# Optimization experiments

Hardware: AMD Instinct MI355X
Metric: run time of the kernel (lower is better)

Reference implementation:

```python
import jax, jax.numpy as jnp
import numpy as np

N, F, D = 32, 1024, 512
H = 2 * D  # dim * ratio
EPS = 1e-5


def batchnorm1d(x, gamma, beta):
    # x: (N, F, L); BatchNorm1d over channel dim F, stats over (N, L) (training mode, biased var)
    mean = jnp.mean(x, axis=(0, 2), keepdims=True)
    var = jnp.var(x, axis=(0, 2), keepdims=True)
    xn = (x - mean) * jax.lax.rsqrt(var + EPS)
    return xn * gamma[None, :, None] + beta[None, :, None]


def setup_inputs() -> dict:
    key = jax.random.key(0)
    ks = jax.random.split(key, 5)
    x = jax.random.normal(ks[0], (N, F, D), dtype=jnp.float32)
    W0 = jax.random.normal(ks[1], (H, D), dtype=jnp.float32) * 0.02  # Linear(D->H) weight (out,in)
    b0 = jnp.zeros((H,), jnp.float32)
    W1 = jax.random.normal(ks[2], (D, H), dtype=jnp.float32) * 0.02  # Linear(H->D)
    b1 = jnp.zeros((D,), jnp.float32)
    Wc = jax.random.normal(ks[3], (F, F), dtype=jnp.float32) * 0.02  # Conv1d k=1 weight (out_ch,in_ch)
    bc = jnp.zeros((F,), jnp.float32)
    ones = jnp.ones((F,), jnp.float32)
    zeros = jnp.zeros((F,), jnp.float32)
    return {
        "x": x,
        "W0": W0, "b0": b0, "g0": ones, "be0": zeros,
        "W1": W1, "b1": b1, "g1": ones, "be1": zeros,
        "gf": ones, "bf": zeros,
        "Wc": Wc, "bc": bc,
        "go": ones, "bo": zeros,
    }


def reference(x, W0, b0, g0, be0, W1, b1, g1, be1, gf, bf, Wc, bc, go, bo):
    # proj_mlp0: Linear(D->H) + BN1d(F)
    v = jnp.einsum('nfd,hd->nfh', x, W0) + b0  # (N, F, H)
    v = batchnorm1d(v, g0, be0)
    # correlation: bmm(v, v^T) -> softsign -> bmm(w, v)
    w = jnp.einsum('nfh,ngh->nfg', v, v)  # (N, F, F)
    w = w / (1.0 + jnp.abs(w))  # softsign
    v = jnp.einsum('nfg,ngh->nfh', w, v)  # (N, F, H)
    # proj_mlp1: Linear(H->D) + BN1d(F)
    v = jnp.einsum('nfh,dh->nfd', v, W1) + b1  # (N, F, D)
    v = batchnorm1d(v, g1, be1)
    # feed_norm(v + x)
    xr = batchnorm1d(v + x, gf, bf)
    # proj_conv: Conv1d(F->F, kernel=1) over channel dim
    v = jnp.einsum('oi,nid->nod', Wc, xr) + bc[None, :, None]
    return batchnorm1d(v + xr, go, bo)
```

## Files before the change

### kernel.cpp

```cpp
#include <hip/hip_runtime.h>
#include <stdint.h>

#define NB 32
#define FC 1024
#define DD 512
#define HH 1024
#define BN_EPS 1e-5f

typedef unsigned short u16;
typedef unsigned int u32;
typedef __attribute__((ext_vector_type(8))) short bf16x8;
typedef __attribute__((ext_vector_type(4))) float f32x4;
typedef __attribute__((ext_vector_type(8))) unsigned short ushort8v;

#define AS1 __attribute__((address_space(1)))
#define AS3 __attribute__((address_space(3)))

__device__ __forceinline__ float b2f(u16 u) {
    union { u32 i; float f; } v;
    v.i = ((u32)u) << 16;
    return v.f;
}
__device__ __forceinline__ u16 f2b(float f) {
    union { float f; u32 i; } v;
    v.f = f;
    const u32 b = v.i;
    return (u16)((b + 0x7FFFu + ((b >> 16) & 1u)) >> 16);
}

__device__ __forceinline__ void gld16(const u16* g, u16* l) {
    __builtin_amdgcn_global_load_lds((const AS1 u32*)g, (AS3 u32*)l, 16, 0, 0);
}

__device__ __forceinline__ void swizzle_tiles(int& mt, int& nt, int& zt) {
    const int gx = gridDim.x, gy = gridDim.y, gz = gridDim.z;
    const int mzTot = gy * gz;
    if ((mzTot & 7) != 0) { nt = blockIdx.x; mt = blockIdx.y; zt = blockIdx.z; return; }
    long lin = ((long)blockIdx.z * gy + blockIdx.y) * gx + blockIdx.x;
    const int slab = mzTot >> 3;
    const int xcd = (int)(lin & 7);
    const long idx = lin >> 3;
    nt = (int)(idx % gx);
    const int mz = (int)(idx / gx) + xcd * slab;
    mt = mz % gy;
    zt = mz / gy;
}

__global__ __launch_bounds__(256) void init_detect(
    float* __restrict__ sp, const u32* __restrict__ x, int* __restrict__ flag)
{
    sp[blockIdx.x * 256 + threadIdx.x] = 0.0f;
    if (blockIdx.x != 0) return;
    __shared__ int cnt[256];
    int c = 0;
    for (int i = threadIdx.x; i < 4096; i += 256) {
        const u32 lo = x[i] & 0xFFFFu;
        const u32 e = (lo >> 7) & 0xFFu;
        if (e >= 0x68u && e <= 0x85u) c++;
    }
    cnt[threadIdx.x] = c;
    __syncthreads();
    for (int s = 128; s > 0; s >>= 1) {
        if (threadIdx.x < (unsigned)s) cnt[threadIdx.x] += cnt[threadIdx.x + s];
        __syncthreads();
    }
    if (threadIdx.x == 0) flag[0] = (cnt[0] > 2048) ? 1 : 0;
}

__global__ __launch_bounds__(256) void fold_bn(
    const float* __restrict__ sp, const u16* __restrict__ gamma,
    const u16* __restrict__ beta, float* __restrict__ ssf, float invCnt)
{
    const int f = blockIdx.x * 256 + threadIdx.x;
    if (f < FC) {
        const float mean = sp[f] * invCnt;
        const float var  = sp[FC + f] * invCnt - mean * mean;
        const float rstd = rsqrtf(var + BN_EPS);
        const float sc   = b2f(gamma[f]) * rstd;
        ssf[f]      = sc;
        ssf[FC + f] = b2f(beta[f]) - mean * sc;
    }
}

__global__ __launch_bounds__(256) void convert_to_bf16(
    const void* __restrict__ src, u16* __restrict__ dst, long n4,
    const int* __restrict__ flag)
{
    const bool isbf = (*flag != 0);
    long i4 = (long)blockIdx.x * blockDim.x + threadIdx.x;
    const long stride = (long)gridDim.x * blockDim.x;
    for (; i4 < n4; i4 += stride) {
        const long i = i4 << 2;
        if (isbf) {
            *(ushort4*)(dst + i) = *(const ushort4*)((const u16*)src + i);
        } else {
            const float4 v = *(const float4*)((const float*)src + i);
            ushort4 o;
            o.x = f2b(v.x); o.y = f2b(v.y); o.z = f2b(v.z); o.w = f2b(v.w);
            *(ushort4*)(dst + i) = o;
        }
    }
}

struct ConvArgs { const void* src[14]; long off[14]; long n4[14]; };
__global__ __launch_bounds__(256) void convert_params(
    ConvArgs a, u16* __restrict__ dst, const int* __restrict__ flag)
{
    const bool isbf = (*flag != 0);
    const long stride = (long)gridDim.x * blockDim.x;
    for (int s = 0; s < 14; ++s) {
        const long n4 = a.n4[s];
        u16* d = dst + a.off[s];
        const void* sp = a.src[s];
        for (long i4 = (long)blockIdx.x * blockDim.x + threadIdx.x; i4 < n4;
             i4 += stride) {
            const long i = i4 << 2;
            if (isbf) {
                *(ushort4*)(d + i) = *(const ushort4*)((const u16*)sp + i);
            } else {
                const float4 v = *(const float4*)((const float*)sp + i);
                ushort4 o;
                o.x = f2b(v.x); o.y = f2b(v.y); o.z = f2b(v.z); o.w = f2b(v.w);
                *(ushort4*)(d + i) = o;
            }
        }
    }
}

template<bool BIAS, bool SOFTSIGN, bool STATS, bool RESID>
__global__ __launch_bounds__(512, 4) void gemm128x256_nt(
    const u16* __restrict__ A, const u16* __restrict__ B,
    const u16* __restrict__ bias, const u16* __restrict__ resid,
    u16* __restrict__ C, float* __restrict__ sp,
    int M, int N, int K, int lda, int ldb, int ldc,
    long sA, long sB, long sC)
{
    extern __shared__ char smem[];

    int mt, nt, zt;
    swizzle_tiles(mt, nt, zt);
    const u16* Ab = A + (long)zt * sA + (long)(mt * 128) * lda;
    const u16* Bb = B + (long)zt * sB + (long)(nt * 256) * ldb;
    C += (long)zt * sC;
    const u16* RP = RESID ? (resid + (long)zt * sC) : nullptr;

    const int tid  = threadIdx.x;
    const int lane = tid & 63;
    const int wv   = tid >> 6;
    const int wrr  = (wv >> 2) * 64;
    const int wc   = (wv & 3) * 64;
    const int lm   = lane & 15;
    const int q    = lane >> 4;

    int aOff[4], bOff[4];
    #pragma unroll
    for (int i = 0; i < 4; ++i) {
        const int r = wrr + i * 16 + lm;
        aOff[i] = r * 64 + ((q ^ ((r >> 1) & 3)) << 4);
    }
    #pragma unroll
    for (int j = 0; j < 4; ++j) {
        const int r = wc + j * 16 + lm;
        bOff[j] = r * 64 + ((q ^ ((r >> 1) & 3)) << 4);
    }

    const int rw = lane >> 2, qs = lane & 3;
    const int rA  = wv * 16 + rw;
    const int rB0 = wv * 32 + rw;
    const int rB1 = wv * 32 + 16 + rw;
    const u16* pA  = Ab + (long)rA  * lda + ((qs ^ ((rA  >> 1) & 3)) << 3);
    const u16* pB0 = Bb + (long)rB0 * ldb + ((qs ^ ((rB0 >> 1) & 3)) << 3);
    const u16* pB1 = Bb + (long)rB1 * ldb + ((qs ^ ((rB1 >> 1) & 3)) << 3);
    const int ldsA  = wv * 1024;
    const int ldsB0 = wv * 2048;
    const int ldsB1 = wv * 2048 + 1024;

#define STAGE(bufOff, kofs) { \
    gld16(pA  + (kofs), (u16*)(smem + (bufOff) + ldsA)); \
    gld16(pB0 + (kofs), (u16*)(smem + (bufOff) + 8192 + ldsB0)); \
    gld16(pB1 + (kofs), (u16*)(smem + (bufOff) + 8192 + ldsB1)); }

    f32x4 acc[4][4] = {};

    const int NT = K >> 5;

    STAGE(0, 0);
    __syncthreads();

    for (int t = 0; t < NT; ++t) {
        const int bo = (t & 1) * 24576;
        const int bn = ((t + 1) & 1) * 24576;
        if (t + 1 < NT) STAGE(bn, (t + 1) * 32);

        bf16x8 a[4], b[4];
        const char* baseA = smem + bo;
        const char* baseB = smem + bo + 8192;
        #pragma unroll
        for (int i = 0; i < 4; ++i) a[i] = *(const bf16x8*)(baseA + aOff[i]);
        #pragma unroll
        for (int j = 0; j < 4; ++j) b[j] = *(const bf16x8*)(baseB + bOff[j]);

        #pragma unroll
        for (int i = 0; i < 4; ++i)
            #pragma unroll
            for (int j = 0; j < 4; ++j)
                acc[i][j] = __builtin_amdgcn_mfma_f32_16x16x32_bf16(
                    a[i], b[j], acc[i][j], 0, 0, 0);

        __syncthreads();
    }

#undef STAGE

    float* rep = (float*)smem + wv * (16 * 65);
    const int rr = lane >> 2;
    const int cg = lane & 3;
    const int m0 = mt * 128;
    const int n0 = nt * 256;
    #pragma unroll
    for (int i = 0; i < 4; ++i) {
        #pragma unroll
        for (int j = 0; j < 4; ++j) {
            const int col = 16 * j + lm;
            const float bj = BIAS ? b2f(bias[n0 + wc + col]) : 0.0f;
            #pragma unroll
            for (int r = 0; r < 4; ++r) {
                float v = acc[i][j][r] + bj;
                if (SOFTSIGN) v = v / (1.0f + fabsf(v));
                rep[(q * 4 + r) * 65 + col] = v;
            }
        }
        const int row = m0 + wrr + 16 * i + rr;
        const float* lr = rep + rr * 65 + cg * 16;
        float4 f0 = *(const float4*)(lr + 0);
        float4 f1 = *(const float4*)(lr + 4);
        float4 f2 = *(const float4*)(lr + 8);
        float4 f3 = *(const float4*)(lr + 12);
        if (RESID) {
            const u16* rp = RP + (long)row * ldc + n0 + wc + cg * 16;
            const ushort8v ra = *(const ushort8v*)rp;
            const ushort8v rb = *(const ushort8v*)(rp + 8);
            f0.x += b2f(ra[0]); f0.y += b2f(ra[1]); f0.z += b2f(ra[2]); f0.w += b2f(ra[3]);
            f1.x += b2f(ra[4]); f1.y += b2f(ra[5]); f1.z += b2f(ra[6]); f1.w += b2f(ra[7]);
            f2.x += b2f(rb[0]); f2.y += b2f(rb[1]); f2.z += b2f(rb[2]); f2.w += b2f(rb[3]);
            f3.x += b2f(rb[4]); f3.y += b2f(rb[5]); f3.z += b2f(rb[6]); f3.w += b2f(rb[7]);
        }
        if (STATS) {
            float s1 = (f0.x + f0.y + f0.z + f0.w) + (f1.x + f1.y + f1.z + f1.w)
                     + (f2.x + f2.y + f2.z + f2.w) + (f3.x + f3.y + f3.z + f3.w);
            float s2 = f0.x*f0.x + f0.y*f0.y + f0.z*f0.z + f0.w*f0.w
                     + f1.x*f1.x + f1.y*f1.y + f1.z*f1.z + f1.w*f1.w
                     + f2.x*f2.x + f2.y*f2.y + f2.z*f2.z + f2.w*f2.w
                     + f3.x*f3.x + f3.y*f3.y + f3.z*f3.z + f3.w*f3.w;
            s1 += __shfl_xor(s1, 1); s1 += __shfl_xor(s1, 2);
            s2 += __shfl_xor(s2, 1); s2 += __shfl_xor(s2, 2);
            if (cg == 0) {
                const int ch = row & (FC - 1);
                atomicAdd(&sp[ch], s1);
                atomicAdd(&sp[FC + ch], s2);
            }
        }
        ushort8v o0, o1;
        o0[0] = f2b(f0.x); o0[1] = f2b(f0.y); o0[2] = f2b(f0.z); o0[3] = f2b(f0.w);
        o0[4] = f2b(f1.x); o0[5] = f2b(f1.y); o0[6] = f2b(f1.z); o0[7] = f2b(f1.w);
        o1[0] = f2b(f2.x); o1[1] = f2b(f2.y); o1[2] = f2b(f2.z); o1[3] = f2b(f2.w);
        o1[4] = f2b(f3.x); o1[5] = f2b(f3.y); o1[6] = f2b(f3.z); o1[7] = f2b(f3.w);
        u16* cp = C + (long)row * ldc + n0 + wc + cg * 16;
        *(ushort8v*)cp = o0;
        *(ushort8v*)(cp + 8) = o1;
    }
}

__global__ __launch_bounds__(256) void transpose_bn_bf16(
    const u16* __restrict__ src, u16* __restrict__ dstT,
    u16* __restrict__ dstI, const float* __restrict__ ssf,
    int R, int Cc, long sS, long sD)
{
    __shared__ u16 t[32][36];
    const int bz = blockIdx.z;
    src  += (long)bz * sS;
    dstI += (long)bz * sS;
    dstT += (long)bz * sD;
    const int c0 = blockIdx.x * 32;
    const int r0 = blockIdx.y * 32;
    const int lx = threadIdx.x & 7;
    const int ly = threadIdx.x >> 3;

    const int r = r0 + ly;
    const float sc = ssf[r];
    const float sh = ssf[FC + r];
    const ushort4 v = *(const ushort4*)(src + (long)r * Cc + c0 + lx * 4);
    ushort4 nv;
    nv.x = f2b(fmaf(b2f(v.x), sc, sh));
    nv.y = f2b(fmaf(b2f(v.y), sc, sh));
    nv.z = f2b(fmaf(b2f(v.z), sc, sh));
    nv.w = f2b(fmaf(b2f(v.w), sc, sh));
    *(ushort4*)(dstI + (long)r * Cc + c0 + lx * 4) = nv;
    *(ushort4*)&t[ly][lx * 4] = nv;

    __syncthreads();

    const int oc = c0 + ly;
    ushort4 o;
    o.x = t[lx * 4 + 0][ly];
    o.y = t[lx * 4 + 1][ly];
    o.z = t[lx * 4 + 2][ly];
    o.w = t[lx * 4 + 3][ly];
    *(ushort4*)(dstT + (long)oc * R + r0 + lx * 4) = o;
}

template<bool ADD, bool STATS>
__global__ __launch_bounds__(256) void bn_apply(
    const u16* __restrict__ src, const void* __restrict__ add,
    const int* __restrict__ addflag,
    const float* __restrict__ ss, void* __restrict__ dst,
    const int* __restrict__ outflag, long total4, int lcShift,
    float* __restrict__ sp)
{
    const bool addf32 = ADD && (addflag != nullptr) && (*addflag == 0);
    const bool outf32 = (outflag != nullptr) && (*outflag == 0);
    long i4 = (long)blockIdx.x * blockDim.x + threadIdx.x;
    const long stride = (long)gridDim.x * blockDim.x;
    for (; i4 < total4; i4 += stride) {
        const long i = i4 << 2;
        const int c = (int)((i >> lcShift) & (FC - 1));
        const float sc = ss[c];
        const float sh = ss[FC + c];
        const ushort4 v = *(const ushort4*)(src + i);
        float o0 = fmaf(b2f(v.x), sc, sh);
        float o1 = fmaf(b2f(v.y), sc, sh);
        float o2 = fmaf(b2f(v.z), sc, sh);
        float o3 = fmaf(b2f(v.w), sc, sh);
        if (ADD) {
            if (addf32) {
                const float4 a = *(const float4*)((const float*)add + i);
                o0 += a.x; o1 += a.y; o2 += a.z; o3 += a.w;
            } else {
                const ushort4 a = *(const ushort4*)((const u16*)add + i);
                o0 += b2f(a.x); o1 += b2f(a.y); o2 += b2f(a.z); o3 += b2f(a.w);
            }
        }
        if (STATS) {
            float s1 = o0 + o1 + o2 + o3;
            float s2 = o0 * o0 + o1 * o1 + o2 * o2 + o3 * o3;
            #pragma unroll
            for (int m = 1; m < 64; m <<= 1) {
                s1 += __shfl_xor(s1, m);
                s2 += __shfl_xor(s2, m);
            }
            if ((threadIdx.x & 63) == 0) {
                atomicAdd(&sp[c], s1);
                atomicAdd(&sp[FC + c], s2);
            }
        }
        if (outf32) {
            float4 o; o.x = o0; o.y = o1; o.z = o2; o.w = o3;
            *(float4*)((float*)dst + i) = o;
        } else {
            ushort4 o;
            o.x = f2b(o0); o.y = f2b(o1); o.z = f2b(o2); o.w = f2b(o3);
            *(ushort4*)((u16*)dst + i) = o;
        }
    }
}

extern "C" void kernel_launch(void* const* d_in, const int* in_sizes, int n_in,
                              void* d_out, int out_size, void* d_ws, size_t ws_size,
                              hipStream_t stream)
{
    const size_t MiB = (size_t)1 << 20;
    const long sFH = (long)FC * HH;
    const long sFF = (long)FC * FC;
    const long sFD = (long)FC * DD;
    const long PE  = (long)NB * FC * DD;

    const size_t GLDS = 49152;
    static bool s_attr = false;
    if (!s_attr) {
        s_attr = true;
        hipFuncSetAttribute(reinterpret_cast<const void*>(&gemm128x256_nt<true, false, true, false>),
                            hipFuncAttributeMaxDynamicSharedMemorySize, (int)GLDS);
        hipFuncSetAttribute(reinterpret_cast<const void*>(&gemm128x256_nt<false, true, false, false>),
                            hipFuncAttributeMaxDynamicSharedMemorySize, (int)GLDS);
        hipFuncSetAttribute(reinterpret_cast<const void*>(&gemm128x256_nt<false, false, false, false>),
                            hipFuncAttributeMaxDynamicSharedMemorySize, (int)GLDS);
        hipFuncSetAttribute(reinterpret_cast<const void*>(&gemm128x256_nt<true, false, true, true>),
                            hipFuncAttributeMaxDynamicSharedMemorySize, (int)GLDS);
    }

    long off[16];
    long cur = 0;
    for (int i = 1; i < 15; ++i) { off[i] = cur; cur += ((long)in_sizes[i] + 7) & ~7L; }
    const size_t paramBytes = (size_t)cur * 2;

    int cb = 32;
    while (cb > 1 &&
           64 * MiB + (size_t)cb * 6 * MiB + paramBytes + 65536 > ws_size)
        cb >>= 1;

    u16* V   = (u16*)d_ws;
    u16* VT  = (u16*)((char*)d_ws + 64 * MiB);
    u16* WW  = VT + (long)cb * sFH;
    u16* V2  = WW + (long)cb * sFF;
    u16* WC  = V2 + (long)cb * sFH;
    char* tail = (char*)(WC + cur);
    tail = (char*)(((uintptr_t)tail + 255) & ~(uintptr_t)255);
    float* SP0  = (float*)tail;
    float* SP1  = SP0 + 2 * FC;
    float* SP2  = SP1 + 2 * FC;
    float* SP3  = SP2 + 2 * FC;
    float* SSF  = SP3 + 2 * FC;
    int*   FLAG = (int*)(SSF + 2 * FC);
    u16* VX  = (u16*)d_out;
    u16* XB  = (u16*)d_out + PE;
    u16* V4  = V;
    u16* XRT = V + PE;

    const dim3 blk(256);
    const dim3 blk512(512);
    const dim3 egrid(4096);

    init_detect<<<dim3(32), blk, 0, stream>>>(SP0, (const u32*)d_in[0], FLAG);
    ConvArgs ca;
    for (int i = 1; i < 15; ++i) {
        ca.src[i - 1] = d_in[i];
        ca.off[i - 1] = off[i];
        ca.n4[i - 1]  = (long)in_sizes[i] / 4;
    }
    convert_params<<<dim3(256), blk, 0, stream>>>(ca, WC, FLAG);
    convert_to_bf16<<<dim3(1024), blk, 0, stream>>>(d_in[0], XB, PE / 4, FLAG);

    const u16* W0c = WC + off[1];
    const u16* b0c = WC + off[2];
    const u16* g0c = WC + off[3];
    const u16* be0c = WC + off[4];
    const u16* W1c = WC + off[5];
    const u16* b1c = WC + off[6];
    const u16* g1c = WC + off[7];
    const u16* be1c = WC + off[8];
    const u16* gfc = WC + off[9];
    const u16* bfc = WC + off[10];
    const u16* Wcc = WC + off[11];
    const u16* bcc = WC + off[12];
    const u16* goc = WC + off[13];
    const u16* boc = WC + off[14];

    gemm128x256_nt<true, false, true, false><<<dim3(HH / 256, (NB * FC) / 128, 1), blk512, GLDS, stream>>>(
        XB, W0c, b0c, nullptr, V, SP0, NB * FC, HH, DD, DD, DD, HH, 0, 0, 0);
    fold_bn<<<dim3(4), blk, 0, stream>>>(SP0, g0c, be0c, SSF, 1.0f / (float)(NB * HH));

    for (int bz0 = 0; bz0 < NB; bz0 += cb) {
        const int c = (NB - bz0 < cb) ? (NB - bz0) : cb;
        transpose_bn_bf16<<<dim3(HH / 32, FC / 32, c), blk, 0, stream>>>(
            V + bz0 * sFH, VT, V + bz0 * sFH, SSF, FC, HH, sFH, sFH);
        gemm128x256_nt<false, true, false, false><<<dim3(FC / 256, FC / 128, c), blk512, GLDS, stream>>>(
            V + bz0 * sFH, V + bz0 * sFH, nullptr, nullptr, WW, nullptr,
            FC, FC, HH, HH, HH, FC, sFH, sFH, sFF);
        gemm128x256_nt<false, false, false, false><<<dim3(HH / 256, FC / 128, c), blk512, GLDS, stream>>>(
            WW, VT, nullptr, nullptr, V2, nullptr,
            FC, HH, FC, FC, FC, HH, sFF, sFH, sFH);
        gemm128x256_nt<true, false, true, false><<<dim3(DD / 256, (c * FC) / 128, 1), blk512, GLDS, stream>>>(
            V2, W1c, b1c, nullptr, VX + bz0 * sFD, SP1,
            c * FC, DD, HH, HH, HH, DD, 0, 0, 0);
    }
    fold_bn<<<dim3(4), blk, 0, stream>>>(SP1, g1c, be1c, SSF, 1.0f / (float)(NB * DD));

    bn_apply<true, true><<<egrid, blk, 0, stream>>>(
        VX, XB, nullptr, SSF, VX, nullptr, PE / 4, 9, SP2);
    fold_bn<<<dim3(4), blk, 0, stream>>>(SP2, gfc, bfc, SSF, 1.0f / (float)(NB * DD));

    transpose_bn_bf16<<<dim3(DD / 32, FC / 32, NB), blk, 0, stream>>>(
        VX, XRT, VX, SSF, FC, DD, sFD, sFD);

    gemm128x256_nt<true, false, true, true><<<dim3(DD / 256, FC / 128, NB), blk512, GLDS, stream>>>(
        Wcc, XRT, bcc, VX, V4, SP3, FC, DD, FC, FC, FC, DD, 0, sFD, sFD);
    fold_bn<<<dim3(4), blk, 0, stream>>>(SP3, goc, boc, SSF, 1.0f / (float)(NB * DD));

    bn_apply<false, false><<<egrid, blk, 0, stream>>>(
        V4, nullptr, nullptr, SSF, d_out, FLAG, PE / 4, 9, nullptr);
}
```

Measured before the change: 605.6 us.

## Derive feed-norm stats algebraically and fuse residual BN pass into transpose

Measured after the change: 591.5 us. 2.3% less time.

```diff
diff --git a/kernel.cpp b/kernel.cpp
--- a/kernel.cpp
+++ b/kernel.cpp
@@ -82,22 +82,64 @@
     }
 }
 
-__global__ __launch_bounds__(256) void convert_to_bf16(
+__global__ __launch_bounds__(256) void fold2_bn(
+    const float* __restrict__ sp1, const float* __restrict__ spx,
+    const u16* __restrict__ g1, const u16* __restrict__ be1,
+    const u16* __restrict__ gf, const u16* __restrict__ bf_,
+    float* __restrict__ ssd, float cnt)
+{
+    const int f = blockIdx.x * 256 + threadIdx.x;
+    if (f >= FC) return;
+    const float inv  = 1.0f / cnt;
+    const float S1v = sp1[f], S2v = sp1[FC + f], Sxv = sp1[2 * FC + f];
+    const float mean1 = S1v * inv;
+    const float var1  = S2v * inv - mean1 * mean1;
+    const float sc1   = b2f(g1[f]) * rsqrtf(var1 + BN_EPS);
+    const float sh1   = b2f(be1[f]) - mean1 * sc1;
+    ssd[f]      = sc1;
+    ssd[FC + f] = sh1;
+    const float S1x = spx[f], S2x = spx[FC + f];
+    const float sums = sc1 * S1v + cnt * sh1 + S1x;
+    const float sss  = sc1 * sc1 * S2v + 2.f * sc1 * sh1 * S1v
+                     + cnt * sh1 * sh1 + 2.f * sc1 * Sxv
+                     + 2.f * sh1 * S1x + S2x;
+    const float means = sums * inv;
+    const float vars  = sss * inv - means * means;
+    const float scf   = b2f(gf[f]) * rsqrtf(vars + BN_EPS);
+    const float shf   = b2f(bf_[f]) - means * scf;
+    ssd[2 * FC + f] = scf;
+    ssd[3 * FC + f] = shf;
+}
+
+__global__ __launch_bounds__(256) void convert_x_stats(
     const void* __restrict__ src, u16* __restrict__ dst, long n4,
-    const int* __restrict__ flag)
+    const int* __restrict__ flag, float* __restrict__ spx)
 {
     const bool isbf = (*flag != 0);
     long i4 = (long)blockIdx.x * blockDim.x + threadIdx.x;
     const long stride = (long)gridDim.x * blockDim.x;
     for (; i4 < n4; i4 += stride) {
         const long i = i4 << 2;
+        ushort4 o;
         if (isbf) {
-            *(ushort4*)(dst + i) = *(const ushort4*)((const u16*)src + i);
+            o = *(const ushort4*)((const u16*)src + i);
         } else {
             const float4 v = *(const float4*)((const float*)src + i);
-            ushort4 o;
             o.x = f2b(v.x); o.y = f2b(v.y); o.z = f2b(v.z); o.w = f2b(v.w);
-            *(ushort4*)(dst + i) = o;
+        }
+        *(ushort4*)(dst + i) = o;
+        const float a = b2f(o.x), b = b2f(o.y), c = b2f(o.z), d = b2f(o.w);
+        float s1 = a + b + c + d;
+        float s2 = a * a + b * b + c * c + d * d;
+        #pragma unroll
+        for (int m = 1; m < 64; m <<= 1) {
+            s1 += __shfl_xor(s1, m);
+            s2 += __shfl_xor(s2, m);
+        }
+        if ((threadIdx.x & 63) == 0) {
+            const int ch = (int)((i >> 9) & (FC - 1));
+            atomicAdd(&spx[ch], s1);
+            atomicAdd(&spx[FC + ch], s2);
         }
     }
 }
@@ -127,7 +169,7 @@
     }
 }
 
-template<bool BIAS, bool SOFTSIGN, bool STATS, bool RESID>
+template<bool BIAS, bool SOFTSIGN, bool STATS, bool RESID, bool XSTAT>
 __global__ __launch_bounds__(512, 4) void gemm128x256_nt(
     const u16* __restrict__ A, const u16* __restrict__ B,
     const u16* __restrict__ bias, const u16* __restrict__ resid,
@@ -142,7 +184,7 @@
     const u16* Ab = A + (long)zt * sA + (long)(mt * 128) * lda;
     const u16* Bb = B + (long)zt * sB + (long)(nt * 256) * ldb;
     C += (long)zt * sC;
-    const u16* RP = RESID ? (resid + (long)zt * sC) : nullptr;
+    const u16* RP = (RESID || XSTAT) ? (resid + (long)zt * sC) : nullptr;
 
     const int tid  = threadIdx.x;
     const int lane = tid & 63;
@@ -236,10 +278,13 @@
         float4 f1 = *(const float4*)(lr + 4);
         float4 f2 = *(const float4*)(lr + 8);
         float4 f3 = *(const float4*)(lr + 12);
+        ushort8v ra, rb;
+        if (RESID || XSTAT) {
+            const u16* rp = RP + (long)row * ldc + n0 + wc + cg * 16;
+            ra = *(const ushort8v*)rp;
+            rb = *(const ushort8v*)(rp + 8);
+        }
         if (RESID) {
-            const u16* rp = RP + (long)row * ldc + n0 + wc + cg * 16;
-            const ushort8v ra = *(const ushort8v*)rp;
-            const ushort8v rb = *(const ushort8v*)(rp + 8);
             f0.x += b2f(ra[0]); f0.y += b2f(ra[1]); f0.z += b2f(ra[2]); f0.w += b2f(ra[3]);
             f1.x += b2f(ra[4]); f1.y += b2f(ra[5]); f1.z += b2f(ra[6]); f1.w += b2f(ra[7]);
             f2.x += b2f(rb[0]); f2.y += b2f(rb[1]); f2.z += b2f(rb[2]); f2.w += b2f(rb[3]);
@@ -252,12 +297,21 @@
                      + f1.x*f1.x + f1.y*f1.y + f1.z*f1.z + f1.w*f1.w
                      + f2.x*f2.x + f2.y*f2.y + f2.z*f2.z + f2.w*f2.w
                      + f3.x*f3.x + f3.y*f3.y + f3.z*f3.z + f3.w*f3.w;
+            float sxv = 0.0f;
+            if (XSTAT) {
+                sxv = f0.x*b2f(ra[0]) + f0.y*b2f(ra[1]) + f0.z*b2f(ra[2]) + f0.w*b2f(ra[3])
+                    + f1.x*b2f(ra[4]) + f1.y*b2f(ra[5]) + f1.z*b2f(ra[6]) + f1.w*b2f(ra[7])
+                    + f2.x*b2f(rb[0]) + f2.y*b2f(rb[1]) + f2.z*b2f(rb[2]) + f2.w*b2f(rb[3])
+                    + f3.x*b2f(rb[4]) + f3.y*b2f(rb[5]) + f3.z*b2f(rb[6]) + f3.w*b2f(rb[7]);
+            }
             s1 += __shfl_xor(s1, 1); s1 += __shfl_xor(s1, 2);
             s2 += __shfl_xor(s2, 1); s2 += __shfl_xor(s2, 2);
+            if (XSTAT) { sxv += __shfl_xor(sxv, 1); sxv += __shfl_xor(sxv, 2); }
             if (cg == 0) {
                 const int ch = row & (FC - 1);
                 atomicAdd(&sp[ch], s1);
                 atomicAdd(&sp[FC + ch], s2);
+                if (XSTAT) atomicAdd(&sp[2 * FC + ch], sxv);
             }
         }
         ushort8v o0, o1;
@@ -309,15 +363,55 @@
     *(ushort4*)(dstT + (long)oc * R + r0 + lx * 4) = o;
 }
 
-template<bool ADD, bool STATS>
+__global__ __launch_bounds__(256) void transpose_bn2_bf16(
+    const u16* __restrict__ v3, const u16* __restrict__ x,
+    u16* __restrict__ dstT, u16* __restrict__ dstI,
+    const float* __restrict__ ssd, int R, int Cc, long sS, long sD)
+{
+    __shared__ u16 t[32][36];
+    const int bz = blockIdx.z;
+    v3   += (long)bz * sS;
+    x    += (long)bz * sS;
+    dstI += (long)bz * sS;
+    dstT += (long)bz * sD;
+    const int c0 = blockIdx.x * 32;
+    const int r0 = blockIdx.y * 32;
+    const int lx = threadIdx.x & 7;
+    const int ly = threadIdx.x >> 3;
+
+    const int r = r0 + ly;
+    const float sc1 = ssd[r];
+    const float sh1 = ssd[FC + r];
+    const float scf = ssd[2 * FC + r];
+    const float shf = ssd[3 * FC + r];
+    const long base = (long)r * Cc + c0 + lx * 4;
+    const ushort4 v  = *(const ushort4*)(v3 + base);
+    const ushort4 xv = *(const ushort4*)(x + base);
+    ushort4 nv;
+    float s;
+    s = fmaf(b2f(v.x), sc1, sh1) + b2f(xv.x); nv.x = f2b(fmaf(s, scf, shf));
+    s = fmaf(b2f(v.y), sc1, sh1) + b2f(xv.y); nv.y = f2b(fmaf(s, scf, shf));
+    s = fmaf(b2f(v.z), sc1, sh1) + b2f(xv.z); nv.z = f2b(fmaf(s, scf, shf));
+    s = fmaf(b2f(v.w), sc1, sh1) + b2f(xv.w); nv.w = f2b(fmaf(s, scf, shf));
+    *(ushort4*)(dstI + base) = nv;
+    *(ushort4*)&t[ly][lx * 4] = nv;
+
+    __syncthreads();
+
+    const int oc = c0 + ly;
+    ushort4 o;
+    o.x = t[lx * 4 + 0][ly];
+    o.y = t[lx * 4 + 1][ly];
+    o.z = t[lx * 4 + 2][ly];
+    o.w = t[lx * 4 + 3][ly];
+    *(ushort4*)(dstT + (long)oc * R + r0 + lx * 4) = o;
+}
+
 __global__ __launch_bounds__(256) void bn_apply(
-    const u16* __restrict__ src, const void* __restrict__ add,
-    const int* __restrict__ addflag,
-    const float* __restrict__ ss, void* __restrict__ dst,
-    const int* __restrict__ outflag, long total4, int lcShift,
-    float* __restrict__ sp)
-{
-    const bool addf32 = ADD && (addflag != nullptr) && (*addflag == 0);
+    const u16* __restrict__ src, const float* __restrict__ ss,
+    void* __restrict__ dst, const int* __restrict__ outflag,
+    long total4, int lcShift)
+{
     const bool outf32 = (outflag != nullptr) && (*outflag == 0);
     long i4 = (long)blockIdx.x * blockDim.x + threadIdx.x;
     const long stride = (long)gridDim.x * blockDim.x;
@@ -327,32 +421,10 @@
         const float sc = ss[c];
         const float sh = ss[FC + c];
         const ushort4 v = *(const ushort4*)(src + i);
-        float o0 = fmaf(b2f(v.x), sc, sh);
-        float o1 = fmaf(b2f(v.y), sc, sh);
-        float o2 = fmaf(b2f(v.z), sc, sh);
-        float o3 = fmaf(b2f(v.w), sc, sh);
-        if (ADD) {
-            if (addf32) {
-                const float4 a = *(const float4*)((const float*)add + i);
-                o0 += a.x; o1 += a.y; o2 += a.z; o3 += a.w;
-            } else {
-                const ushort4 a = *(const ushort4*)((const u16*)add + i);
-                o0 += b2f(a.x); o1 += b2f(a.y); o2 += b2f(a.z); o3 += b2f(a.w);
-            }
-        }
-        if (STATS) {
-            float s1 = o0 + o1 + o2 + o3;
-            float s2 = o0 * o0 + o1 * o1 + o2 * o2 + o3 * o3;
-            #pragma unroll
-            for (int m = 1; m < 64; m <<= 1) {
-                s1 += __shfl_xor(s1, m);
-                s2 += __shfl_xor(s2, m);
-            }
-            if ((threadIdx.x & 63) == 0) {
-                atomicAdd(&sp[c], s1);
-                atomicAdd(&sp[FC + c], s2);
-            }
-        }
+        const float o0 = fmaf(b2f(v.x), sc, sh);
+        const float o1 = fmaf(b2f(v.y), sc, sh);
+        const float o2 = fmaf(b2f(v.z), sc, sh);
+        const float o3 = fmaf(b2f(v.w), sc, sh);
         if (outf32) {
             float4 o; o.x = o0; o.y = o1; o.z = o2; o.w = o3;
             *(float4*)((float*)dst + i) = o;
@@ -378,13 +450,15 @@
     static bool s_attr = false;
     if (!s_attr) {
         s_attr = true;
-        hipFuncSetAttribute(reinterpret_cast<const void*>(&gemm128x256_nt<true, false, true, false>),
+        hipFuncSetAttribute(reinterpret_cast<const void*>(&gemm128x256_nt<true, false, true, false, false>),
                             hipFuncAttributeMaxDynamicSharedMemorySize, (int)GLDS);
-        hipFuncSetAttribute(reinterpret_cast<const void*>(&gemm128x256_nt<false, true, false, false>),
+        hipFuncSetAttribute(reinterpret_cast<const void*>(&gemm128x256_nt<false, true, false, false, false>),
                             hipFuncAttributeMaxDynamicSharedMemorySize, (int)GLDS);
-        hipFuncSetAttribute(reinterpret_cast<const void*>(&gemm128x256_nt<false, false, false, false>),
+        hipFuncSetAttribute(reinterpret_cast<const void*>(&gemm128x256_nt<false, false, false, false, false>),
                             hipFuncAttributeMaxDynamicSharedMemorySize, (int)GLDS);
-        hipFuncSetAttribute(reinterpret_cast<const void*>(&gemm128x256_nt<true, false, true, true>),
+        hipFuncSetAttribute(reinterpret_cast<const void*>(&gemm128x256_nt<true, false, true, false, true>),
+                            hipFuncAttributeMaxDynamicSharedMemorySize, (int)GLDS);
+        hipFuncSetAttribute(reinterpret_cast<const void*>(&gemm128x256_nt<true, false, true, true, false>),
                             hipFuncAttributeMaxDynamicSharedMemorySize, (int)GLDS);
     }
 
@@ -395,7 +469,7 @@
 
     int cb = 32;
     while (cb > 1 &&
-           64 * MiB + (size_t)cb * 6 * MiB + paramBytes + 65536 > ws_size)
+           64 * MiB + (size_t)cb * 6 * MiB + paramBytes + 131072 > ws_size)
         cb >>= 1;
 
     u16* V   = (u16*)d_ws;
@@ -407,10 +481,11 @@
     tail = (char*)(((uintptr_t)tail + 255) & ~(uintptr_t)255);
     float* SP0  = (float*)tail;
     float* SP1  = SP0 + 2 * FC;
-    float* SP2  = SP1 + 2 * FC;
-    float* SP3  = SP2 + 2 * FC;
+    float* SPX  = SP1 + 3 * FC;
+    float* SP3  = SPX + 2 * FC;
     float* SSF  = SP3 + 2 * FC;
-    int*   FLAG = (int*)(SSF + 2 * FC);
+    float* SSD  = SSF + 2 * FC;
+    int*   FLAG = (int*)(SSD + 4 * FC);
     u16* VX  = (u16*)d_out;
     u16* XB  = (u16*)d_out + PE;
     u16* V4  = V;
@@ -420,7 +495,7 @@
     const dim3 blk512(512);
     const dim3 egrid(4096);
 
-    init_detect<<<dim3(32), blk, 0, stream>>>(SP0, (const u32*)d_in[0], FLAG);
+    init_detect<<<dim3(36), blk, 0, stream>>>(SP0, (const u32*)d_in[0], FLAG);
     ConvArgs ca;
     for (int i = 1; i < 15; ++i) {
         ca.src[i - 1] = d_in[i];
@@ -428,7 +503,7 @@
         ca.n4[i - 1]  = (long)in_sizes[i] / 4;
     }
     convert_params<<<dim3(256), blk, 0, stream>>>(ca, WC, FLAG);
-    convert_to_bf16<<<dim3(1024), blk, 0, stream>>>(d_in[0], XB, PE / 4, FLAG);
+    convert_x_stats<<<dim3(1024), blk, 0, stream>>>(d_in[0], XB, PE / 4, FLAG, SPX);
 
     const u16* W0c = WC + off[1];
     const u16* b0c = WC + off[2];
@@ -445,7 +520,7 @@
     const u16* goc = WC + off[13];
     const u16* boc = WC + off[14];
 
-    gemm128x256_nt<true, false, true, false><<<dim3(HH / 256, (NB * FC) / 128, 1), blk512, GLDS, stream>>>(
+    gemm128x256_nt<true, false, true, false, false><<<dim3(HH / 256, (NB * FC) / 128, 1), blk512, GLDS, stream>>>(
         XB, W0c, b0c, nullptr, V, SP0, NB * FC, HH, DD, DD, DD, HH, 0, 0, 0);
     fold_bn<<<dim3(4), blk, 0, stream>>>(SP0, g0c, be0c, SSF, 1.0f / (float)(NB * HH));
 
@@ -453,29 +528,26 @@
         const int c = (NB - bz0 < cb) ? (NB - bz0) : cb;
         transpose_bn_bf16<<<dim3(HH / 32, FC / 32, c), blk, 0, stream>>>(
             V + bz0 * sFH, VT, V + bz0 * sFH, SSF, FC, HH, sFH, sFH);
-        gemm128x256_nt<false, true, false, false><<<dim3(FC / 256, FC / 128, c), blk512, GLDS, stream>>>(
+        gemm128x256_nt<false, true, false, false, false><<<dim3(FC / 256, FC / 128, c), blk512, GLDS, stream>>>(
             V + bz0 * sFH, V + bz0 * sFH, nullptr, nullptr, WW, nullptr,
             FC, FC, HH, HH, HH, FC, sFH, sFH, sFF);
-        gemm128x256_nt<false, false, false, false><<<dim3(HH / 256, FC / 128, c), blk512, GLDS, stream>>>(
+        gemm128x256_nt<false, false, false, false, false><<<dim3(HH / 256, FC / 128, c), blk512, GLDS, stream>>>(
             WW, VT, nullptr, nullptr, V2, nullptr,
             FC, HH, FC, FC, FC, HH, sFF, sFH, sFH);
-        gemm128x256_nt<true, false, true, false><<<dim3(DD / 256, (c * FC) / 128, 1), blk512, GLDS, stream>>>(
-            V2, W1c, b1c, nullptr, VX + bz0 * sFD, SP1,
+        gemm128x256_nt<true, false, true, false, true><<<dim3(DD / 256, (c * FC) / 128, 1), blk512, GLDS, stream>>>(
+            V2, W1c, b1c, XB + bz0 * sFD, VX + bz0 * sFD, SP1,
             c * FC, DD, HH, HH, HH, DD, 0, 0, 0);
     }
-    fold_bn<<<dim3(4), blk, 0, stream>>>(SP1, g1c, be1c, SSF, 1.0f / (float)(NB * DD));
-
-    bn_apply<true, true><<<egrid, blk, 0, stream>>>(
-        VX, XB, nullptr, SSF, VX, nullptr, PE / 4, 9, SP2);
-    fold_bn<<<dim3(4), blk, 0, stream>>>(SP2, gfc, bfc, SSF, 1.0f / (float)(NB * DD));
-
-    transpose_bn_bf16<<<dim3(DD / 32, FC / 32, NB), blk, 0, stream>>>(
-        VX, XRT, VX, SSF, FC, DD, sFD, sFD);
-
-    gemm128x256_nt<true, false, true, true><<<dim3(DD / 256, FC / 128, NB), blk512, GLDS, stream>>>(
+
+    fold2_bn<<<dim3(4), blk, 0, stream>>>(SP1, SPX, g1c, be1c, gfc, bfc,
+                                          SSD, (float)(NB * DD));
+
+    transpose_bn2_bf16<<<dim3(DD / 32, FC / 32, NB), blk, 0, stream>>>(
+        VX, XB, XRT, VX, SSD, FC, DD, sFD, sFD);
+
+    gemm128x256_nt<true, false, true, true, false><<<dim3(DD / 256, FC / 128, NB), blk512, GLDS, stream>>>(
         Wcc, XRT, bcc, VX, V4, SP3, FC, DD, FC, FC, FC, DD, 0, sFD, sFD);
     fold_bn<<<dim3(4), blk, 0, stream>>>(SP3, goc, boc, SSF, 1.0f / (float)(NB * DD));
 
-    bn_apply<false, false><<<egrid, blk, 0, stream>>>(
-        V4, nullptr, nullptr, SSF, d_out, FLAG, PE / 4, 9, nullptr);
-}
+    bn_apply<<<egrid, blk, 0, stream>>>(V4, SSF, d_out, FLAG, PE / 4, 9);
+}
```
